# Performance work log

Hardware: AMD Instinct MI355X
Metric: run time of the kernel (lower is better)

Reference implementation:

```python
import jax, jax.numpy as jnp
import numpy as np

N = 20000      # number of nodes
K = 32         # neighbors per node (per edge type)
D_FEAT = 128   # feature dim


def setup_inputs() -> dict:
    key = jax.random.key(0)
    k1, k2, k3 = jax.random.split(key, 3)
    feat = jax.random.normal(k1, (N, D_FEAT), dtype=jnp.float32)
    sim_idx = jax.random.randint(k2, (N, K), 0, N)
    cor_idx = jax.random.randint(k3, (N, K), 0, N)
    return {"feat": feat, "sim_idx": sim_idx, "cor_idx": cor_idx}


def _coattention(Dm, Qm):
    # Dm, Qm: [N, K, d]
    L = jnp.einsum('nkd,njd->nkj', Dm, Qm)          # [N, K, K]
    AC = jax.nn.softmax(L, axis=-1)                  # softmax over Q-neighbors
    AS = jax.nn.softmax(jnp.swapaxes(L, 1, 2), axis=-1)  # softmax over D-neighbors
    CQ = jnp.einsum('nkj,njd->nkd', AC, Qm)          # [N, K, d]
    CD = jnp.einsum('nkj,njd->nkd', AS, jnp.concatenate([Dm, CQ], axis=-1))  # [N, K, 2d]
    return jnp.concatenate([Qm, CD], axis=-1)        # [N, K, 3d]


def reference(feat, sim_idx, cor_idx):
    # mode == 'cor': D <- sim edges, Q <- cor edges (dropout=0 => identity)
    Dm = feat[sim_idx]   # [N, K, d] gather
    Qm = feat[cor_idx]   # [N, K, d] gather
    h = _coattention(Dm, Qm)                          # [N, K, 3d]
    n, k, td = h.shape
    # AvgPool1d(kernel=3, stride=3) over last dim -> [N, K, d]
    h = h.reshape(n, k, td // 3, 3).mean(axis=-1)
    h_neigh = h.mean(axis=1)                          # mean over K neighbors -> [N, d]
    return feat + h_neigh
```

## Files before the change

kernel.cpp:

```cpp
#include <hip/hip_runtime.h>

#define KN 32
#define DF 128
#define WPB 2

typedef float  f32x16 __attribute__((ext_vector_type(16)));
typedef float  f32x2  __attribute__((ext_vector_type(2)));
typedef short  s16x8  __attribute__((ext_vector_type(8)));

union ldsu { int4 i; s16x8 v; };

__device__ __forceinline__ unsigned int pk_bf16(float lo, float hi) {
    unsigned int r;
    asm("v_cvt_pk_bf16_f32 %0, %1, %2" : "=v"(r) : "v"(lo), "v"(hi));
    return r;
}
__device__ __forceinline__ float ex2(float x) {
    float r; asm("v_exp_f32 %0, %1" : "=v"(r) : "v"(x)); return r;
}
__device__ __forceinline__ float bflo(unsigned int u) { return __uint_as_float(u << 16); }
__device__ __forceinline__ float bfhi(unsigned int u) { return __uint_as_float(u & 0xffff0000u); }

__device__ __forceinline__ void gll16(const void* g, void* l) {
    __builtin_amdgcn_global_load_lds(
        (const __attribute__((address_space(1))) unsigned int*)g,
        (__attribute__((address_space(3))) unsigned int*)l,
        16, 0, 0);
}

__global__ __launch_bounds__(256)
void cvt_kernel(const float* __restrict__ f, unsigned short* __restrict__ bf,
                unsigned char* __restrict__ f8, int n8) {
    const int i = blockIdx.x * blockDim.x + threadIdx.x;
    if (i >= n8) return;
    const float s = 1.20112240872f;
    float4 x0 = ((const float4*)f)[2 * i];
    float4 x1 = ((const float4*)f)[2 * i + 1];
    int4 b;
    b.x = (int)pk_bf16(s * x0.x, s * x0.y); b.y = (int)pk_bf16(s * x0.z, s * x0.w);
    b.z = (int)pk_bf16(s * x1.x, s * x1.y); b.w = (int)pk_bf16(s * x1.z, s * x1.w);
    ((int4*)bf)[i] = b;
    int p0 = __builtin_amdgcn_cvt_pk_fp8_f32(x0.x, x0.y, 0, false);
    p0     = __builtin_amdgcn_cvt_pk_fp8_f32(x0.z, x0.w, p0, true);
    int p1 = __builtin_amdgcn_cvt_pk_fp8_f32(x1.x, x1.y, 0, false);
    p1     = __builtin_amdgcn_cvt_pk_fp8_f32(x1.z, x1.w, p1, true);
    ((int2*)f8)[i] = make_int2(p0, p1);
}

__global__ __launch_bounds__(WPB * 64, 2)
void coattn_kernel(const float* __restrict__ feat,
                   const unsigned char* __restrict__ featbf,
                   const unsigned char* __restrict__ feat8,
                   const int* __restrict__ sim_idx,
                   const int* __restrict__ cor_idx,
                   float* __restrict__ out, int nnodes) {
    __shared__ int4 Ls[WPB][2][KN][8];
    const int wv = threadIdx.x >> 6;
    const int l  = threadIdx.x & 63;
    const int c  = l & 31;
    const int h  = l >> 5;
    const int g  = l >> 3;
    const int m  = l & 7;
    const int n  = blockIdx.x * WPB + wv;
    if (n >= nnodes) return;

    const int si = sim_idx[n * KN + c];
    const int ci = cor_idx[n * KN + c];
    const unsigned pidx = ((unsigned)ci << 16) | (unsigned)si;
    const unsigned swz = (unsigned)(((m ^ g) & 7) * 16);

    f32x16 acc  = {0,0,0,0,0,0,0,0,0,0,0,0,0,0,0,0};
    f32x16 accT = {0,0,0,0,0,0,0,0,0,0,0,0,0,0,0,0};
    unsigned spk[4];
    #pragma unroll
    for (int t = 0; t < 4; ++t) spk[t] = (unsigned)__shfl((int)pidx, 8 * t + g, 64);
    #pragma unroll
    for (int H = 0; H < 2; ++H) {
        const unsigned hoff = (unsigned)(H * 128) + swz;
        #pragma unroll
        for (int t = 0; t < 4; ++t)
            gll16(featbf + (spk[t] & 0xffffu) * 256u + hoff, (void*)&Ls[wv][0][8 * t][0]);
        #pragma unroll
        for (int t = 0; t < 4; ++t)
            gll16(featbf + (spk[t] >> 16) * 256u + hoff, (void*)&Ls[wv][1][8 * t][0]);
        asm volatile("s_waitcnt vmcnt(4)" ::: "memory");
        __builtin_amdgcn_sched_barrier(0);
        s16x8 fD[4], fQ[4];
        #pragma unroll
        for (int sp = 0; sp < 4; ++sp) {
            union ldsu u; u.i = Ls[wv][0][c][(sp * 2 + h) ^ (c & 7)];
            fD[sp] = u.v;
        }
        asm volatile("s_waitcnt vmcnt(0)" ::: "memory");
        __builtin_amdgcn_sched_barrier(0);
        #pragma unroll
        for (int sp = 0; sp < 4; ++sp) {
            union ldsu u; u.i = Ls[wv][1][c][(sp * 2 + h) ^ (c & 7)];
            fQ[sp] = u.v;
        }
        #pragma unroll
        for (int sp = 0; sp < 4; ++sp) {
            acc  = __builtin_amdgcn_mfma_f32_32x32x16_bf16(fD[sp], fQ[sp], acc,  0, 0, 0);
            accT = __builtin_amdgcn_mfma_f32_32x32x16_bf16(fQ[sp], fD[sp], accT, 0, 0, 0);
        }
        asm volatile("s_waitcnt lgkmcnt(0)" ::: "memory");
        __builtin_amdgcn_sched_barrier(0);
    }

    float mx = acc[0];
    #pragma unroll
    for (int p = 1; p < 16; ++p) mx = fmaxf(mx, acc[p]);
    mx = fmaxf(mx, __shfl_xor(mx, 32, 64));
    const float mxf = bfhi(pk_bf16(0.f, mx));
    float z = 0.f;
    #pragma unroll
    for (int p = 0; p < 16; ++p) z += ex2(acc[p] - mxf);
    z += __shfl_xor(z, 32, 64);
    const unsigned pcol = pk_bf16(1.0f / z, mxf);

    float rm = accT[0];
    #pragma unroll
    for (int p = 1; p < 16; ++p) rm = fmaxf(rm, accT[p]);
    rm = fmaxf(rm, __shfl_xor(rm, 32, 64));
    const float rmf = bfhi(pk_bf16(0.f, rm));
    float rs = 0.f;
    #pragma unroll
    for (int p = 0; p < 16; ++p) rs += ex2(accT[p] - rmf);
    rs += __shfl_xor(rs, 32, 64);

    float w = 0.f;
    #pragma unroll
    for (int p = 0; p < 16; ++p) {
        const int jp = (p & 3) + 8 * (p >> 2) + 4 * h;
        const unsigned pc = (unsigned)__shfl((int)pcol, jp, 64);
        w += ex2(accT[p] - bfhi(pc)) * bflo(pc);
    }
    w += __shfl_xor(w, 32, 64);

    const unsigned prow = pk_bf16(w / rs, rmf);
    float v = 0.f;
    #pragma unroll
    for (int p = 0; p < 16; ++p) {
        const int kp = (p & 3) + 8 * (p >> 2) + 4 * h;
        const unsigned pr = (unsigned)__shfl((int)prow, kp, 64);
        v += ex2(acc[p] - bfhi(pr)) * bflo(pr);
    }
    v += __shfl_xor(v, 32, 64);

    const unsigned pwv = pk_bf16(v, w);
    f32x2 sQ2[2] = {{0.f,0.f},{0.f,0.f}};
    f32x2 sD2[2] = {{0.f,0.f},{0.f,0.f}};
    f32x2 sC2[2] = {{0.f,0.f},{0.f,0.f}};
    #pragma unroll
    for (int t = 0; t < 16; ++t) {
        const int b = h * 16 + t;
        const unsigned pi = (unsigned)__shfl((int)pidx, b, 64);
        const unsigned pv = (unsigned)__shfl((int)pwv,  b, 64);
        const float wb = bfhi(pv);
        const float vb = bflo(pv);
        const unsigned int da = *(const unsigned int*)(feat8 + ((pi & 0xffffu) << 7) + 4u * c);
        const unsigned int dq = *(const unsigned int*)(feat8 + ((pi >> 16) << 7) + 4u * c);
        f32x2 a01 = __builtin_amdgcn_cvt_pk_f32_fp8((int)da, false);
        f32x2 a23 = __builtin_amdgcn_cvt_pk_f32_fp8((int)da, true);
        f32x2 q01 = __builtin_amdgcn_cvt_pk_f32_fp8((int)dq, false);
        f32x2 q23 = __builtin_amdgcn_cvt_pk_f32_fp8((int)dq, true);
        const f32x2 wb2 = {wb, wb};
        const f32x2 vb2 = {vb, vb};
        sQ2[0] += q01;                sQ2[1] += q23;
        sD2[0] = wb2 * a01 + sD2[0];  sD2[1] = wb2 * a23 + sD2[1];
        sC2[0] = vb2 * q01 + sC2[0];  sC2[1] = vb2 * q23 + sC2[1];
    }
    #pragma unroll
    for (int i = 0; i < 2; ++i) {
        sQ2[i][0] += __shfl_xor(sQ2[i][0], 32, 64); sQ2[i][1] += __shfl_xor(sQ2[i][1], 32, 64);
        sD2[i][0] += __shfl_xor(sD2[i][0], 32, 64); sD2[i][1] += __shfl_xor(sD2[i][1], 32, 64);
        sC2[i][0] += __shfl_xor(sC2[i][0], 32, 64); sC2[i][1] += __shfl_xor(sC2[i][1], 32, 64);
    }

    float* const S_sh = (float*)Ls[wv];
    if (h == 0) {
        *(float4*)&S_sh[0 * DF + 4 * c] = make_float4(sQ2[0][0], sQ2[0][1], sQ2[1][0], sQ2[1][1]);
        *(float4*)&S_sh[1 * DF + 4 * c] = make_float4(sD2[0][0], sD2[0][1], sD2[1][0], sD2[1][1]);
        *(float4*)&S_sh[2 * DF + 4 * c] = make_float4(sC2[0][0], sC2[0][1], sC2[1][0], sC2[1][1]);
    }
    asm volatile("s_waitcnt lgkmcnt(0)" ::: "memory");
    const float h0 = S_sh[6 * l + 0] + S_sh[6 * l + 1] + S_sh[6 * l + 2];
    const float h1 = S_sh[6 * l + 3] + S_sh[6 * l + 4] + S_sh[6 * l + 5];
    const float* fr = feat + (long)n * DF;
    const float o0 = fr[2 * l + 0] + h0 * (1.0f / 96.0f);
    const float o1 = fr[2 * l + 1] + h1 * (1.0f / 96.0f);
    *(float2*)&out[(long)n * DF + 2 * l] = make_float2(o0, o1);
}

#define RP 136
__global__ __launch_bounds__(64, 2)
void coattn_v4(const float* __restrict__ feat,
               const int* __restrict__ sim_idx,
               const int* __restrict__ cor_idx,
               float* __restrict__ out, int nnodes) {
    __shared__ unsigned char lds[2 * KN * RP];
    unsigned char* Ab8 = lds;
    unsigned char* Bb8 = lds + KN * RP;
    float* S_sh = (float*)lds;
    const int n = blockIdx.x;
    const int l = threadIdx.x;
    const int c = l & 31;
    const int h = l >> 5;
    const int si = sim_idx[n * KN + c];
    const int ci = cor_idx[n * KN + c];
    const float* Dr = feat + (long)si * DF;
    const float* Qr = feat + (long)ci * DF;
    f32x16 acc  = {0,0,0,0,0,0,0,0,0,0,0,0,0,0,0,0};
    f32x16 accT = {0,0,0,0,0,0,0,0,0,0,0,0,0,0,0,0};
    #pragma unroll
    for (int s = 0; s < 8; ++s) {
        const int d0 = s * 16 + h * 8;
        float4 a0 = *(const float4*)(Dr + d0);
        float4 a1 = *(const float4*)(Dr + d0 + 4);
        float4 b0 = *(const float4*)(Qr + d0);
        float4 b1 = *(const float4*)(Qr + d0 + 4);
        union { s16x8 v8; unsigned int u[4]; } ua, ub;
        ua.u[0] = pk_bf16(a0.x, a0.y); ua.u[1] = pk_bf16(a0.z, a0.w);
        ua.u[2] = pk_bf16(a1.x, a1.y); ua.u[3] = pk_bf16(a1.z, a1.w);
        ub.u[0] = pk_bf16(b0.x, b0.y); ub.u[1] = pk_bf16(b0.z, b0.w);
        ub.u[2] = pk_bf16(b1.x, b1.y); ub.u[3] = pk_bf16(b1.z, b1.w);
        acc  = __builtin_amdgcn_mfma_f32_32x32x16_bf16(ua.v8, ub.v8, acc,  0, 0, 0);
        accT = __builtin_amdgcn_mfma_f32_32x32x16_bf16(ub.v8, ua.v8, accT, 0, 0, 0);
        int pa0 = __builtin_amdgcn_cvt_pk_fp8_f32(a0.x, a0.y, 0, false);
        pa0     = __builtin_amdgcn_cvt_pk_fp8_f32(a0.z, a0.w, pa0, true);
        int pa1 = __builtin_amdgcn_cvt_pk_fp8_f32(a1.x, a1.y, 0, false);
        pa1     = __builtin_amdgcn_cvt_pk_fp8_f32(a1.z, a1.w, pa1, true);
        int pb0 = __builtin_amdgcn_cvt_pk_fp8_f32(b0.x, b0.y, 0, false);
        pb0     = __builtin_amdgcn_cvt_pk_fp8_f32(b0.z, b0.w, pb0, true);
        int pb1 = __builtin_amdgcn_cvt_pk_fp8_f32(b1.x, b1.y, 0, false);
        pb1     = __builtin_amdgcn_cvt_pk_fp8_f32(b1.z, b1.w, pb1, true);
        *(int2*)(Ab8 + c * RP + d0) = make_int2(pa0, pa1);
        *(int2*)(Bb8 + c * RP + d0) = make_int2(pb0, pb1);
    }
    float mx = acc[0];
    #pragma unroll
    for (int p = 1; p < 16; ++p) mx = fmaxf(mx, acc[p]);
    mx = fmaxf(mx, __shfl_xor(mx, 32, 64));
    float z = 0.f;
    #pragma unroll
    for (int p = 0; p < 16; ++p) z += __expf(acc[p] - mx);
    z += __shfl_xor(z, 32, 64);
    const float invZ = 1.0f / z;
    float rm = accT[0];
    #pragma unroll
    for (int p = 1; p < 16; ++p) rm = fmaxf(rm, accT[p]);
    rm = fmaxf(rm, __shfl_xor(rm, 32, 64));
    float rs = 0.f;
    #pragma unroll
    for (int p = 0; p < 16; ++p) rs += __expf(accT[p] - rm);
    rs += __shfl_xor(rs, 32, 64);
    const float invR = 1.0f / rs;
    float w = 0.f;
    #pragma unroll
    for (int p = 0; p < 16; ++p) {
        const int jp = (p & 3) + 8 * (p >> 2) + 4 * h;
        w += __expf(accT[p] - __shfl(mx, jp, 64)) * __shfl(invZ, jp, 64);
    }
    w += __shfl_xor(w, 32, 64);
    const float u = w * invR;
    float v = 0.f;
    #pragma unroll
    for (int p = 0; p < 16; ++p) {
        const int kp = (p & 3) + 8 * (p >> 2) + 4 * h;
        v += __expf(acc[p] - __shfl(rm, kp, 64)) * __shfl(u, kp, 64);
    }
    v += __shfl_xor(v, 32, 64);
    __syncthreads();
    float sQ[4] = {0,0,0,0}, sD[4] = {0,0,0,0}, sC[4] = {0,0,0,0};
    const unsigned char* Abase = Ab8 + h * 16 * RP + 4 * c;
    const unsigned char* Bbase = Bb8 + h * 16 * RP + 4 * c;
    #pragma unroll
    for (int t = 0; t < 16; ++t) {
        const int b = h * 16 + t;
        const float wb = __shfl(w, b, 64);
        const float vb = __shfl(v, b, 64);
        const unsigned int da = *(const unsigned int*)(Abase + t * RP);
        const unsigned int dq = *(const unsigned int*)(Bbase + t * RP);
        f32x2 a01 = __builtin_amdgcn_cvt_pk_f32_fp8((int)da, false);
        f32x2 a23 = __builtin_amdgcn_cvt_pk_f32_fp8((int)da, true);
        f32x2 q01 = __builtin_amdgcn_cvt_pk_f32_fp8((int)dq, false);
        f32x2 q23 = __builtin_amdgcn_cvt_pk_f32_fp8((int)dq, true);
        sQ[0] += q01[0]; sQ[1] += q01[1]; sQ[2] += q23[0]; sQ[3] += q23[1];
        sD[0] = fmaf(wb, a01[0], sD[0]); sD[1] = fmaf(wb, a01[1], sD[1]);
        sD[2] = fmaf(wb, a23[0], sD[2]); sD[3] = fmaf(wb, a23[1], sD[3]);
        sC[0] = fmaf(vb, q01[0], sC[0]); sC[1] = fmaf(vb, q01[1], sC[1]);
        sC[2] = fmaf(vb, q23[0], sC[2]);
        sC[3] = fmaf(vb, q23[1], sC[3]);
    }
    #pragma unroll
    for (int i = 0; i < 4; ++i) {
        sQ[i] += __shfl_xor(sQ[i], 32, 64);
        sD[i] += __shfl_xor(sD[i], 32, 64);
        sC[i] += __shfl_xor(sC[i], 32, 64);
    }
    __syncthreads();
    if (h == 0) {
        *(float4*)&S_sh[0 * DF + 4 * c] = make_float4(sQ[0], sQ[1], sQ[2], sQ[3]);
        *(float4*)&S_sh[1 * DF + 4 * c] = make_float4(sD[0], sD[1], sD[2], sD[3]);
        *(float4*)&S_sh[2 * DF + 4 * c] = make_float4(sC[0], sC[1], sC[2], sC[3]);
    }
    __syncthreads();
    const float h0 = S_sh[6 * l + 0] + S_sh[6 * l + 1] + S_sh[6 * l + 2];
    const float h1 = S_sh[6 * l + 3] + S_sh[6 * l + 4] + S_sh[6 * l + 5];
    const float* fr = feat + (long)n * DF;
    const float o0 = fr[2 * l + 0] + h0 * (1.0f / 96.0f);
    const float o1 = fr[2 * l + 1] + h1 * (1.0f / 96.0f);
    *(float2*)&out[(long)n * DF + 2 * l] = make_float2(o0, o1);
}

extern "C" void kernel_launch(void* const* d_in, const int* in_sizes, int n_in,
                              void* d_out, int out_size, void* d_ws, size_t ws_size,
                              hipStream_t stream) {
    const float* feat = (const float*)d_in[0];
    const int* sim    = (const int*)d_in[1];
    const int* cor    = (const int*)d_in[2];
    float* out        = (float*)d_out;
    const int nnodes  = in_sizes[0] / DF;
    const size_t nfeat = (size_t)nnodes * DF;
    const size_t need  = nfeat * 2 + nfeat;

    if (ws_size >= need) {
        unsigned short* featbf = (unsigned short*)d_ws;
        unsigned char*  feat8  = (unsigned char*)d_ws + nfeat * 2;
        const int n8 = (int)(nfeat / 8);
        hipLaunchKernelGGL(cvt_kernel, dim3((n8 + 255) / 256), dim3(256), 0, stream,
                           feat, featbf, feat8, n8);
        const int blocks = (nnodes + WPB - 1) / WPB;
        hipLaunchKernelGGL(coattn_kernel, dim3(blocks), dim3(WPB * 64), 0, stream,
                           feat, (const unsigned char*)featbf, feat8, sim, cor, out, nnodes);
    } else {
        hipLaunchKernelGGL(coattn_v4, dim3(nnodes), dim3(64), 0, stream,
                           feat, sim, cor, out, nnodes);
    }
}
```

Measured before the change: 57.11 us.

## Prefetch fp8 neighbor rows during MFMA phase and halve LDS staging buffer

Moves the 32 fp8 gathers used in the weighted-sum phase so they are issued early, via inline asm, while the second-half bf16 tiles are still loading, and holds the results in registers until after the softmax. The LDS staging buffer shrinks to one tile per wave, so D and Q halves are loaded one after another into the same slot and overlapped with MFMAs. The aim is to hide gather latency and reduce LDS use, which may allow more occupancy. The cost is more serialized waits on the bf16 loads and higher register pressure from 32 in-flight load results.

```diff
diff --git a/kernel.cpp b/kernel.cpp
--- a/kernel.cpp
+++ b/kernel.cpp
@@ -54,7 +54,7 @@
                    const int* __restrict__ sim_idx,
                    const int* __restrict__ cor_idx,
                    float* __restrict__ out, int nnodes) {
-    __shared__ int4 Ls[WPB][2][KN][8];
+    __shared__ int4 Ls[WPB][KN][8];
     const int wv = threadIdx.x >> 6;
     const int l  = threadIdx.x & 63;
     const int c  = l & 31;
@@ -74,37 +74,69 @@
     unsigned spk[4];
     #pragma unroll
     for (int t = 0; t < 4; ++t) spk[t] = (unsigned)__shfl((int)pidx, 8 * t + g, 64);
-    #pragma unroll
-    for (int H = 0; H < 2; ++H) {
-        const unsigned hoff = (unsigned)(H * 128) + swz;
-        #pragma unroll
-        for (int t = 0; t < 4; ++t)
-            gll16(featbf + (spk[t] & 0xffffu) * 256u + hoff, (void*)&Ls[wv][0][8 * t][0]);
-        #pragma unroll
-        for (int t = 0; t < 4; ++t)
-            gll16(featbf + (spk[t] >> 16) * 256u + hoff, (void*)&Ls[wv][1][8 * t][0]);
-        asm volatile("s_waitcnt vmcnt(4)" ::: "memory");
-        __builtin_amdgcn_sched_barrier(0);
-        s16x8 fD[4], fQ[4];
-        #pragma unroll
-        for (int sp = 0; sp < 4; ++sp) {
-            union ldsu u; u.i = Ls[wv][0][c][(sp * 2 + h) ^ (c & 7)];
-            fD[sp] = u.v;
-        }
-        asm volatile("s_waitcnt vmcnt(0)" ::: "memory");
-        __builtin_amdgcn_sched_barrier(0);
-        #pragma unroll
-        for (int sp = 0; sp < 4; ++sp) {
-            union ldsu u; u.i = Ls[wv][1][c][(sp * 2 + h) ^ (c & 7)];
-            fQ[sp] = u.v;
-        }
-        #pragma unroll
-        for (int sp = 0; sp < 4; ++sp) {
-            acc  = __builtin_amdgcn_mfma_f32_32x32x16_bf16(fD[sp], fQ[sp], acc,  0, 0, 0);
-            accT = __builtin_amdgcn_mfma_f32_32x32x16_bf16(fQ[sp], fD[sp], accT, 0, 0, 0);
-        }
-        asm volatile("s_waitcnt lgkmcnt(0)" ::: "memory");
-        __builtin_amdgcn_sched_barrier(0);
+
+    #pragma unroll
+    for (int t = 0; t < 4; ++t)
+        gll16(featbf + (spk[t] & 0xffffu) * 256u + swz, (void*)&Ls[wv][8 * t][0]);
+    asm volatile("s_waitcnt vmcnt(0)" ::: "memory");
+    __builtin_amdgcn_sched_barrier(0);
+    s16x8 fD[4], fQ[4];
+    #pragma unroll
+    for (int sp = 0; sp < 4; ++sp) {
+        union ldsu u; u.i = Ls[wv][c][(sp * 2 + h) ^ (c & 7)]; fD[sp] = u.v;
+    }
+    asm volatile("s_waitcnt lgkmcnt(0)" ::: "memory");
+    __builtin_amdgcn_sched_barrier(0);
+    #pragma unroll
+    for (int t = 0; t < 4; ++t)
+        gll16(featbf + (spk[t] >> 16) * 256u + swz, (void*)&Ls[wv][8 * t][0]);
+    asm volatile("s_waitcnt vmcnt(0)" ::: "memory");
+    __builtin_amdgcn_sched_barrier(0);
+    #pragma unroll
+    for (int sp = 0; sp < 4; ++sp) {
+        union ldsu u; u.i = Ls[wv][c][(sp * 2 + h) ^ (c & 7)]; fQ[sp] = u.v;
+    }
+    asm volatile("s_waitcnt lgkmcnt(0)" ::: "memory");
+    __builtin_amdgcn_sched_barrier(0);
+
+    #pragma unroll
+    for (int t = 0; t < 4; ++t)
+        gll16(featbf + (spk[t] & 0xffffu) * 256u + 128u + swz, (void*)&Ls[wv][8 * t][0]);
+    #pragma unroll
+    for (int sp = 0; sp < 4; ++sp) {
+        acc  = __builtin_amdgcn_mfma_f32_32x32x16_bf16(fD[sp], fQ[sp], acc,  0, 0, 0);
+        accT = __builtin_amdgcn_mfma_f32_32x32x16_bf16(fQ[sp], fD[sp], accT, 0, 0, 0);
+    }
+    asm volatile("s_waitcnt vmcnt(0)" ::: "memory");
+    __builtin_amdgcn_sched_barrier(0);
+    #pragma unroll
+    for (int sp = 0; sp < 4; ++sp) {
+        union ldsu u; u.i = Ls[wv][c][(sp * 2 + h) ^ (c & 7)]; fD[sp] = u.v;
+    }
+    asm volatile("s_waitcnt lgkmcnt(0)" ::: "memory");
+    __builtin_amdgcn_sched_barrier(0);
+    #pragma unroll
+    for (int t = 0; t < 4; ++t)
+        gll16(featbf + (spk[t] >> 16) * 256u + 128u + swz, (void*)&Ls[wv][8 * t][0]);
+    unsigned da[16], dq[16];
+    #pragma unroll
+    for (int t = 0; t < 16; ++t) {
+        const unsigned pi = (unsigned)__shfl((int)pidx, h * 16 + t, 64);
+        const unsigned char* pD = feat8 + ((pi & 0xffffu) << 7) + 4u * c;
+        const unsigned char* pQ = feat8 + ((pi >> 16) << 7) + 4u * c;
+        asm volatile("global_load_dword %0, %1, off" : "=v"(da[t]) : "v"(pD) : "memory");
+        asm volatile("global_load_dword %0, %1, off" : "=v"(dq[t]) : "v"(pQ) : "memory");
+    }
+    asm volatile("s_waitcnt vmcnt(32)" ::: "memory");
+    __builtin_amdgcn_sched_barrier(0);
+    #pragma unroll
+    for (int sp = 0; sp < 4; ++sp) {
+        union ldsu u; u.i = Ls[wv][c][(sp * 2 + h) ^ (c & 7)]; fQ[sp] = u.v;
+    }
+    #pragma unroll
+    for (int sp = 0; sp < 4; ++sp) {
+        acc  = __builtin_amdgcn_mfma_f32_32x32x16_bf16(fD[sp], fQ[sp], acc,  0, 0, 0);
+        accT = __builtin_amdgcn_mfma_f32_32x32x16_bf16(fQ[sp], fD[sp], accT, 0, 0, 0);
     }
 
     float mx = acc[0];
@@ -148,22 +180,21 @@
     v += __shfl_xor(v, 32, 64);
 
     const unsigned pwv = pk_bf16(v, w);
+    asm volatile("s_waitcnt vmcnt(0)" ::: "memory");
+    __builtin_amdgcn_sched_barrier(0);
     f32x2 sQ2[2] = {{0.f,0.f},{0.f,0.f}};
     f32x2 sD2[2] = {{0.f,0.f},{0.f,0.f}};
     f32x2 sC2[2] = {{0.f,0.f},{0.f,0.f}};
     #pragma unroll
     for (int t = 0; t < 16; ++t) {
         const int b = h * 16 + t;
-        const unsigned pi = (unsigned)__shfl((int)pidx, b, 64);
-        const unsigned pv = (unsigned)__shfl((int)pwv,  b, 64);
+        const unsigned pv = (unsigned)__shfl((int)pwv, b, 64);
         const float wb = bfhi(pv);
         const float vb = bflo(pv);
-        const unsigned int da = *(const unsigned int*)(feat8 + ((pi & 0xffffu) << 7) + 4u * c);
-        const unsigned int dq = *(const unsigned int*)(feat8 + ((pi >> 16) << 7) + 4u * c);
-        f32x2 a01 = __builtin_amdgcn_cvt_pk_f32_fp8((int)da, false);
-        f32x2 a23 = __builtin_amdgcn_cvt_pk_f32_fp8((int)da, true);
-        f32x2 q01 = __builtin_amdgcn_cvt_pk_f32_fp8((int)dq, false);
-        f32x2 q23 = __builtin_amdgcn_cvt_pk_f32_fp8((int)dq, true);
+        f32x2 a01 = __builtin_amdgcn_cvt_pk_f32_fp8((int)da[t], false);
+        f32x2 a23 = __builtin_amdgcn_cvt_pk_f32_fp8((int)da[t], true);
+        f32x2 q01 = __builtin_amdgcn_cvt_pk_f32_fp8((int)dq[t], false);
+        f32x2 q23 = __builtin_amdgcn_cvt_pk_f32_fp8((int)dq[t], true);
         const f32x2 wb2 = {wb, wb};
         const f32x2 vb2 = {vb, vb};
         sQ2[0] += q01;                sQ2[1] += q23;
```

After: 59.56 us. +4.3%, slower.
